# Kernel tuning notes

Measured on AMD Instinct MI355X. Metric: run time of the kernel, lower is better.

The kernel has to match this reference:

```python
import jax, jax.numpy as jnp
import numpy as np

B = 4          # number of point clouds
N = 16384      # points per cloud
RATIO = 0.25
S = int(N * RATIO)   # FPS samples per cloud (fps never duplicates, unique() only sorts)
R = 0.08
K = 32               # max_num_neighbors
BIG = jnp.float32(1e30)


def fps_one(pts):
    """Farthest point sampling on one cloud. pts: [N,3] -> idx [S] (start at 0, random_start=False)."""
    def body(carry, _):
        dists, last = carry
        d = jnp.sum((pts - pts[last]) ** 2, axis=-1)          # [N]
        dists = jnp.minimum(dists, d)
        nxt = jnp.argmax(dists).astype(jnp.int32)
        return (dists, nxt), nxt
    init = (jnp.full((pts.shape[0],), BIG, jnp.float32), jnp.int32(0))
    _, rest = jax.lax.scan(body, init, None, length=S - 1)
    return jnp.concatenate([jnp.zeros((1,), jnp.int32), rest])


def ball_query_one(src, dst):
    """For each dst point pick up to K nearest src points within radius R.
    src: [N,3], dst: [S,3] -> (idx [S,K] int32, valid [S,K] bool)."""
    d2 = jnp.sum((dst[:, None, :] - src[None, :, :]) ** 2, axis=-1)  # [S,N]
    masked = jnp.where(d2 <= R * R, d2, BIG)
    neg_vals, idx = jax.lax.top_k(-masked, K)                        # K smallest distances
    valid = neg_vals > -BIG * 0.5
    return idx.astype(jnp.int32), valid


def setup_inputs() -> dict:
    key = jax.random.key(0)
    k1, _ = jax.random.split(key)
    node_coord_src = jax.random.uniform(k1, (B * N, 3), dtype=jnp.float32)
    batch_src = (jnp.arange(B * N) // N).astype(jnp.int64)
    return {"node_coord_src": node_coord_src, "batch_src": batch_src}


def reference(node_coord_src, batch_src):
    pts = node_coord_src.reshape(B, N, 3)
    # --- FPS + torch.unique (which only sorts, indices are distinct) ---
    fps_idx = jax.vmap(fps_one)(pts)                 # [B,S] local indices
    fps_idx = jnp.sort(fps_idx, axis=-1)
    dst = jnp.take_along_axis(pts, fps_idx[..., None], axis=1)   # [B,S,3]
    # --- radius ball query (padded to K with validity mask) ---
    idx, valid = jax.vmap(ball_query_one)(pts, dst)  # [B,S,K]
    # remove self edges: src local index == fps index of the dst node
    valid = valid & (idx != fps_idx[:, :, None])
    # --- globalize indices and flatten ---
    boff = jnp.arange(B, dtype=jnp.int32)[:, None, None]
    edge_src = (idx + boff * N).reshape(-1)
    edge_dst = jnp.broadcast_to(jnp.arange(S, dtype=jnp.int32)[None, :, None] + boff * S, (B, S, K)).reshape(-1)
    edge_mask = valid.reshape(-1)
    degree = valid.sum(axis=-1).reshape(-1).astype(jnp.int32)    # scatter_add of ones == per-dst count
    node_coord_dst = dst.reshape(-1, 3)
    batch_dst = jnp.repeat(jnp.arange(B, dtype=jnp.int32), S)
    node_dst_idx = (fps_idx + jnp.arange(B, dtype=jnp.int32)[:, None] * N).reshape(-1)
    return (node_coord_dst, edge_src, edge_dst, edge_mask, degree, batch_dst, node_dst_idx)
```

## Files before the change

kernel.cpp:

```cpp
#include <hip/hip_runtime.h>
#include <hip/hip_bf16.h>

constexpr int B = 4;
constexpr int N = 16384;
constexpr int S = 4096;
constexpr int K = 32;
constexpr float BIG = 1e30f;

constexpr size_t OFF_COORD = 0;
constexpr size_t OFF_ESRC  = (size_t)B * S * 3;
constexpr size_t OFF_EDST  = OFF_ESRC + (size_t)B * S * K;
constexpr size_t OFF_MASK  = OFF_EDST + (size_t)B * S * K;
constexpr size_t OFF_DEG   = OFF_MASK + (size_t)B * S * K;
constexpr size_t OFF_BATCH = OFF_DEG + (size_t)B * S;
constexpr size_t OFF_NIDX  = OFF_BATCH + (size_t)B * S;

#define NT_MS 1024
__global__ __launch_bounds__(NT_MS)
void morton_sort_kernel(const float* __restrict__ pts, float4* __restrict__ sbuf) {
    const int b = blockIdx.x, t = threadIdx.x;
    const int lane = t & 63, wave = t >> 6;
    const float* p = pts + (size_t)b * N * 3;
    float4* sb = sbuf + (size_t)b * N;

    __shared__ unsigned int cnt[8192];
    __shared__ int s_wsum[16];

    for (int i = t; i < 8192; i += NT_MS) cnt[i] = 0u;
    __syncthreads();

    float xx[16], yy[16], zz[16];
    int code[16];
#pragma unroll
    for (int j = 0; j < 16; ++j) {
        int i = t + j * NT_MS;
        float x = p[i * 3 + 0], y = p[i * 3 + 1], z = p[i * 3 + 2];
        xx[j] = x; yy[j] = y; zz[j] = z;
        int xi = min(31, (int)(x * 32.0f));
        int yi = min(31, (int)(y * 32.0f));
        int zi = min(15, (int)(z * 16.0f));
        int c = 0;
#pragma unroll
        for (int k = 0; k < 4; ++k) {
            c |= ((zi >> k) & 1) << (3 * k);
            c |= ((yi >> k) & 1) << (3 * k + 1);
            c |= ((xi >> k) & 1) << (3 * k + 2);
        }
        c |= ((xi >> 4) & 1) << 12;
        c |= ((yi >> 4) & 1) << 13;
        code[j] = c;
        atomicAdd(&cnt[c >> 1], (c & 1) ? 0x10000u : 1u);
    }
    __syncthreads();

    unsigned int w[8];
    int tot = 0;
#pragma unroll
    for (int k = 0; k < 8; ++k) {
        w[k] = cnt[t * 8 + k];
        tot += (int)(w[k] & 0xffffu) + (int)(w[k] >> 16);
    }
    int inc = tot;
#pragma unroll
    for (int off = 1; off < 64; off <<= 1) {
        int v = __shfl_up(inc, off);
        if (lane >= off) inc += v;
    }
    if (lane == 63) s_wsum[wave] = inc;
    __syncthreads();
    int wbase = 0;
#pragma unroll
    for (int q = 0; q < 16; ++q) {
        int v = s_wsum[q];
        if (q < wave) wbase += v;
    }
    int excl = wbase + inc - tot;
#pragma unroll
    for (int k = 0; k < 8; ++k) {
        unsigned int c0 = (unsigned int)excl;
        unsigned int c1 = c0 + (w[k] & 0xffffu);
        cnt[t * 8 + k] = c0 | (c1 << 16);
        excl = (int)(c1 + (w[k] >> 16));
    }
    __syncthreads();

#pragma unroll
    for (int j = 0; j < 16; ++j) {
        int i = t + j * NT_MS;
        int c = code[j];
        unsigned int old = atomicAdd(&cnt[c >> 1], (c & 1) ? 0x10000u : 1u);
        int pos = (c & 1) ? (int)(old >> 16) : (int)(old & 0xffffu);
        sb[pos] = make_float4(xx[j], yy[j], zz[j], __int_as_float(i));
    }
}

#define NT_FP 1024
#define CPT 16

__global__ __launch_bounds__(NT_FP, 4)
void fps_pruned_kernel(const float* __restrict__ pts, const float4* __restrict__ sbuf,
                       int* __restrict__ seq) {
    const int b = blockIdx.x, t = threadIdx.x;
    const int lane = t & 63, wave = t >> 6;
    const float* p = pts + (size_t)b * N * 3;
    const float4* sb = sbuf + (size_t)b * N;

    float px[CPT], py[CPT], pz[CPT], dd[CPT];
    unsigned int noi[CPT];
    float blx = BIG, bly = BIG, blz = BIG, bhx = -BIG, bhy = -BIG, bhz = -BIG;
#pragma unroll
    for (int j = 0; j < CPT; ++j) {
        float4 v = sb[t * CPT + j];
        px[j] = v.x; py[j] = v.y; pz[j] = v.z;
        noi[j] = ~(unsigned int)__float_as_int(v.w);
        dd[j] = BIG;
        blx = fminf(blx, v.x); bhx = fmaxf(bhx, v.x);
        bly = fminf(bly, v.y); bhy = fmaxf(bhy, v.y);
        blz = fminf(blz, v.z); bhz = fmaxf(bhz, v.z);
    }
#pragma unroll
    for (int j = 0; j < CPT; ++j)
        asm volatile("" : "+v"(px[j]), "+v"(py[j]), "+v"(pz[j]), "+v"(noi[j]));
    asm volatile("" : "+v"(blx), "+v"(bly), "+v"(blz), "+v"(bhx), "+v"(bhy), "+v"(bhz));

    __shared__ unsigned long long sp[2][NT_FP / 64];

    if (t == 0) seq[b * S + 0] = 0;
    float lx = p[0], ly = p[1], lz = p[2];
    unsigned long long bkey = ((unsigned long long)__float_as_uint(BIG) << 32);

    for (int step = 1; step < S; ++step) {
        float tx = fmaxf(fmaxf(blx - lx, lx - bhx), 0.0f);
        float ty = fmaxf(fmaxf(bly - ly, ly - bhy), 0.0f);
        float tz = fmaxf(fmaxf(blz - lz, lz - bhz), 0.0f);
        float lb = tx * tx + ty * ty + tz * tz;
        float bmax = __uint_as_float((unsigned int)(bkey >> 32));
        if (lb * 0.999998f < bmax) {
            unsigned long long k = 0ull;
#pragma unroll
            for (int j = 0; j < CPT; ++j) {
                float dx = __fsub_rn(px[j], lx);
                float dy = __fsub_rn(py[j], ly);
                float dz = __fsub_rn(pz[j], lz);
                float d  = __fadd_rn(__fadd_rn(__fmul_rn(dx, dx), __fmul_rn(dy, dy)),
                                     __fmul_rn(dz, dz));
                float nd = fminf(dd[j], d);
                dd[j] = nd;
                unsigned long long pk =
                    ((unsigned long long)__float_as_uint(nd) << 32) | noi[j];
                k = (pk > k) ? pk : k;
            }
            bkey = k;
        }
        unsigned long long r = bkey;
#pragma unroll
        for (int off = 32; off >= 1; off >>= 1) {
            unsigned long long o = __shfl_down(r, off);
            r = (o > r) ? o : r;
        }
        if (lane == 0) sp[step & 1][wave] = r;
        __syncthreads();
        unsigned long long g = sp[step & 1][0];
#pragma unroll
        for (int q = 1; q < NT_FP / 64; ++q) {
            unsigned long long o = sp[step & 1][q];
            g = (o > g) ? o : g;
        }
        int wi = (int)(~(unsigned int)g);
        if (t == 0) seq[b * S + step] = wi;
        int wis = __builtin_amdgcn_readfirstlane(wi);
        lx = p[wis * 3 + 0];
        ly = p[wis * 3 + 1];
        lz = p[wis * 3 + 2];
    }
}

#define NT_FPS 512
#define PPT (N / NT_FPS)
#define NWAVE (NT_FPS / 64)
__global__ __launch_bounds__(NT_FPS)
void fps_kernel(const float* __restrict__ pts, int* __restrict__ seq) {
    const int b = blockIdx.x;
    const float* p = pts + (size_t)b * N * 3;
    const int t = threadIdx.x;
    const int lane = t & 63;
    const int wave = t >> 6;
    float px[PPT], py[PPT], pz[PPT], dd[PPT];
    const int base = t * PPT;
#pragma unroll
    for (int j = 0; j < PPT; ++j) {
        px[j] = p[(base + j) * 3 + 0];
        py[j] = p[(base + j) * 3 + 1];
        pz[j] = p[(base + j) * 3 + 2];
        dd[j] = BIG;
    }
#pragma unroll
    for (int j = 0; j < PPT; ++j)
        asm volatile("" : "+v"(px[j]), "+v"(py[j]), "+v"(pz[j]));
    __shared__ unsigned long long s_part[2][NWAVE];
    if (t == 0) seq[b * S + 0] = 0;
    float lx = p[0], ly = p[1], lz = p[2];
    for (int step = 1; step < S; ++step) {
        float bv = -1.0f;
        int bi = 0;
#pragma unroll
        for (int j = 0; j < PPT; ++j) {
            float dx = __fsub_rn(px[j], lx);
            float dy = __fsub_rn(py[j], ly);
            float dz = __fsub_rn(pz[j], lz);
            float d  = __fadd_rn(__fadd_rn(__fmul_rn(dx, dx), __fmul_rn(dy, dy)),
                                 __fmul_rn(dz, dz));
            float nd = fminf(dd[j], d);
            dd[j] = nd;
            if (nd > bv) { bv = nd; bi = base + j; }
        }
        unsigned long long key =
            ((unsigned long long)__float_as_uint(bv) << 32) | (unsigned int)(~bi);
#pragma unroll
        for (int off = 32; off >= 1; off >>= 1) {
            unsigned long long o = __shfl_down(key, off);
            if (o > key) key = o;
        }
        if (lane == 0) s_part[step & 1][wave] = key;
        __syncthreads();
        unsigned long long bk = s_part[step & 1][0];
#pragma unroll
        for (int q = 1; q < NWAVE; ++q) {
            unsigned long long o = s_part[step & 1][q];
            if (o > bk) bk = o;
        }
        int wi = (int)(~(unsigned int)bk);
        if (t == 0) seq[b * S + step] = wi;
        int wis = __builtin_amdgcn_readfirstlane(wi);
        lx = p[wis * 3 + 0];
        ly = p[wis * 3 + 1];
        lz = p[wis * 3 + 2];
    }
}

#define NT_SORT 512
__global__ __launch_bounds__(NT_SORT)
void sort_gather_kernel(const float* __restrict__ pts, const int* __restrict__ seq,
                        int* __restrict__ sorted, float* __restrict__ out) {
    const int b = blockIdx.x;
    const int t = threadIdx.x;
    __shared__ unsigned int bm[N / 32];
    __shared__ int pfx[N / 32];
    __shared__ int s_sorted[S];

    for (int i = t; i < N / 32; i += NT_SORT) bm[i] = 0u;
    __syncthreads();
    for (int i = t; i < S; i += NT_SORT) {
        int v = seq[b * S + i];
        atomicOr(&bm[v >> 5], 1u << (v & 31));
    }
    __syncthreads();

    int myc = __popc(bm[t]);
    pfx[t] = myc;
    __syncthreads();
    for (int off = 1; off < N / 32; off <<= 1) {
        int v = (t >= off) ? pfx[t - off] : 0;
        __syncthreads();
        pfx[t] += v;
        __syncthreads();
    }

    for (int i = t; i < S; i += NT_SORT) {
        int v = seq[b * S + i];
        int w = v >> 5;
        int rank = pfx[w] - __popc(bm[w]) + __popc(bm[w] & ((1u << (v & 31)) - 1u));
        s_sorted[rank] = v;
    }
    __syncthreads();

    for (int r = t; r < S; r += NT_SORT) {
        int v = s_sorted[r];
        int g = b * S + r;
        sorted[g] = v;
        out[OFF_COORD + 3 * (size_t)g + 0] = pts[((size_t)b * N + v) * 3 + 0];
        out[OFF_COORD + 3 * (size_t)g + 1] = pts[((size_t)b * N + v) * 3 + 1];
        out[OFF_COORD + 3 * (size_t)g + 2] = pts[((size_t)b * N + v) * 3 + 2];
        out[OFF_BATCH + g] = (float)b;
        out[OFF_NIDX + g]  = (float)(v + b * N);
    }
}

#define CAP 512
__global__ __launch_bounds__(256)
void ballq_kernel(const float* __restrict__ pts, const int* __restrict__ sorted,
                  float* __restrict__ out) {
    const int w    = threadIdx.x >> 6;
    const int lane = threadIdx.x & 63;
    const int g    = blockIdx.x * 4 + w;
    const int b    = g >> 12;
    const float R2 = (float)(0.08 * 0.08);

    __shared__ float cd2[4][CAP];
    __shared__ int   cidx[4][CAP];
    __shared__ int   coor[4][K];

    const float Dx = out[OFF_COORD + 3 * (size_t)g + 0];
    const float Dy = out[OFF_COORD + 3 * (size_t)g + 1];
    const float Dz = out[OFF_COORD + 3 * (size_t)g + 2];
    const int self = sorted[g];

    const float* p = pts + (size_t)b * N * 3;
    const unsigned long long ltmask = (lane == 63) ? 0x7fffffffffffffffull
                                                   : ((1ull << lane) - 1ull);
    int cnt = 0, oor = 0;
    for (int i0 = 0; i0 < N; i0 += 64) {
        int i = i0 + lane;
        float dx = __fsub_rn(Dx, p[i * 3 + 0]);
        float dy = __fsub_rn(Dy, p[i * 3 + 1]);
        float dz = __fsub_rn(Dz, p[i * 3 + 2]);
        float d2 = __fadd_rn(__fadd_rn(__fmul_rn(dx, dx), __fmul_rn(dy, dy)),
                             __fmul_rn(dz, dz));
        bool in = (d2 <= R2);
        unsigned long long m = __ballot(in);
        if (in) {
            int pos = cnt + __popcll(m & ltmask);
            if (pos < CAP) { cd2[w][pos] = d2; cidx[w][pos] = i; }
        }
        if (oor < K) {
            unsigned long long m2 = ~m;
            if (!in) {
                int p2 = oor + __popcll(m2 & ltmask);
                if (p2 < K) coor[w][p2] = i;
            }
            oor += __popcll(m2);
            if (oor > K) oor = K;
        }
        cnt += __popcll(m);
    }

    const int M  = cnt < CAP ? cnt : CAP;
    const int Mk = M < K ? M : K;
    const size_t eb = (size_t)g * K;
    int deg = 0;
    for (int c = lane; c < M; c += 64) {
        float myd = cd2[w][c];
        int   myi = cidx[w][c];
        int rank = 0;
        for (int j = 0; j < M; ++j) {
            float dj = cd2[w][j];
            int   ij = cidx[w][j];
            rank += (dj < myd || (dj == myd && ij < myi)) ? 1 : 0;
        }
        if (rank < K) {
            bool valid = (myi != self);
            out[OFF_ESRC + eb + rank] = (float)(myi + b * N);
            out[OFF_MASK + eb + rank] = valid ? 1.0f : 0.0f;
            deg += valid ? 1 : 0;
        }
    }
    for (int r = lane; r < K; r += 64) {
        out[OFF_EDST + eb + r] = (float)g;
        if (r >= Mk) {
            out[OFF_ESRC + eb + r] = (float)(coor[w][r - Mk] + b * N);
            out[OFF_MASK + eb + r] = 0.0f;
        }
    }
#pragma unroll
    for (int off = 32; off >= 1; off >>= 1) deg += __shfl_down(deg, off);
    if (lane == 0) out[OFF_DEG + g] = (float)deg;
}

extern "C" void kernel_launch(void* const* d_in, const int* in_sizes, int n_in,
                              void* d_out, int out_size, void* d_ws, size_t ws_size,
                              hipStream_t stream) {
    const float* pts = (const float*)d_in[0];
    float* out = (float*)d_out;

    const size_t sbuf_bytes = (size_t)B * N * sizeof(float4);
    const size_t need = sbuf_bytes + 2 * (size_t)B * S * sizeof(int);

    if (ws_size >= need) {
        float4* sbuf = (float4*)d_ws;
        int* seq    = (int*)((char*)d_ws + sbuf_bytes);
        int* sorted = seq + (size_t)B * S;
        morton_sort_kernel<<<B, NT_MS, 0, stream>>>(pts, sbuf);
        fps_pruned_kernel<<<B, NT_FP, 0, stream>>>(pts, sbuf, seq);
        sort_gather_kernel<<<B, NT_SORT, 0, stream>>>(pts, seq, sorted, out);
        ballq_kernel<<<(B * S) / 4, 256, 0, stream>>>(pts, sorted, out);
    } else {
        int* seq    = (int*)d_ws;
        int* sorted = seq + (size_t)B * S;
        fps_kernel<<<B, NT_FPS, 0, stream>>>(pts, seq);
        sort_gather_kernel<<<B, NT_SORT, 0, stream>>>(pts, seq, sorted, out);
        ballq_kernel<<<(B * S) / 4, 256, 0, stream>>>(pts, sorted, out);
    }
}
```

Before: 5.016 ms.

## Stream FPS point coords from memory instead of registers, skip idle-wave reductions

The pruned FPS kernel no longer keeps each thread's 16 points (x,y,z,index) in registers. It re-reads them as float4 from the sorted buffer whenever the bounding-box test says an update is needed, which cuts register pressure at the cost of repeated global or cache loads per step. Waves where no lane needs an update now skip the shuffle reduction and reuse the cached wave key. The cross-wave final reduction reads the shared partials as 128-bit pairs. The extra memory traffic per step may add latency on the serial critical path.

```diff
diff --git a/kernel.cpp b/kernel.cpp
--- a/kernel.cpp
+++ b/kernel.cpp
@@ -103,31 +103,26 @@
     const int b = blockIdx.x, t = threadIdx.x;
     const int lane = t & 63, wave = t >> 6;
     const float* p = pts + (size_t)b * N * 3;
-    const float4* sb = sbuf + (size_t)b * N;
-
-    float px[CPT], py[CPT], pz[CPT], dd[CPT];
-    unsigned int noi[CPT];
+    const float4* sb = sbuf + (size_t)b * N + (size_t)t * CPT;
+
+    float dd[CPT];
     float blx = BIG, bly = BIG, blz = BIG, bhx = -BIG, bhy = -BIG, bhz = -BIG;
 #pragma unroll
     for (int j = 0; j < CPT; ++j) {
-        float4 v = sb[t * CPT + j];
-        px[j] = v.x; py[j] = v.y; pz[j] = v.z;
-        noi[j] = ~(unsigned int)__float_as_int(v.w);
+        float4 v = sb[j];
         dd[j] = BIG;
         blx = fminf(blx, v.x); bhx = fmaxf(bhx, v.x);
         bly = fminf(bly, v.y); bhy = fmaxf(bhy, v.y);
         blz = fminf(blz, v.z); bhz = fmaxf(bhz, v.z);
     }
-#pragma unroll
-    for (int j = 0; j < CPT; ++j)
-        asm volatile("" : "+v"(px[j]), "+v"(py[j]), "+v"(pz[j]), "+v"(noi[j]));
     asm volatile("" : "+v"(blx), "+v"(bly), "+v"(blz), "+v"(bhx), "+v"(bhy), "+v"(bhz));
 
-    __shared__ unsigned long long sp[2][NT_FP / 64];
+    __shared__ alignas(16) unsigned long long sp[2][NT_FP / 64];
 
     if (t == 0) seq[b * S + 0] = 0;
     float lx = p[0], ly = p[1], lz = p[2];
     unsigned long long bkey = ((unsigned long long)__float_as_uint(BIG) << 32);
+    unsigned long long wkey = bkey;
 
     for (int step = 1; step < S; ++step) {
         float tx = fmaxf(fmaxf(blx - lx, lx - bhx), 0.0f);
@@ -135,36 +130,57 @@
         float tz = fmaxf(fmaxf(blz - lz, lz - bhz), 0.0f);
         float lb = tx * tx + ty * ty + tz * tz;
         float bmax = __uint_as_float((unsigned int)(bkey >> 32));
-        if (lb * 0.999998f < bmax) {
-            unsigned long long k = 0ull;
-#pragma unroll
-            for (int j = 0; j < CPT; ++j) {
-                float dx = __fsub_rn(px[j], lx);
-                float dy = __fsub_rn(py[j], ly);
-                float dz = __fsub_rn(pz[j], lz);
-                float d  = __fadd_rn(__fadd_rn(__fmul_rn(dx, dx), __fmul_rn(dy, dy)),
-                                     __fmul_rn(dz, dz));
-                float nd = fminf(dd[j], d);
-                dd[j] = nd;
-                unsigned long long pk =
-                    ((unsigned long long)__float_as_uint(nd) << 32) | noi[j];
-                k = (pk > k) ? pk : k;
+        bool upd = (lb * 0.999998f < bmax);
+        if (__any(upd)) {
+            if (upd) {
+                unsigned long long k = 0ull;
+#pragma unroll
+                for (int g = 0; g < CPT / 4; ++g) {
+                    float4 v0 = sb[g * 4 + 0];
+                    float4 v1 = sb[g * 4 + 1];
+                    float4 v2 = sb[g * 4 + 2];
+                    float4 v3 = sb[g * 4 + 3];
+#define FPS_PT(V, J)                                                          \
+                    {                                                         \
+                        float dx = __fsub_rn((V).x, lx);                      \
+                        float dy = __fsub_rn((V).y, ly);                      \
+                        float dz = __fsub_rn((V).z, lz);                      \
+                        float d  = __fadd_rn(__fadd_rn(__fmul_rn(dx, dx),     \
+                                   __fmul_rn(dy, dy)), __fmul_rn(dz, dz));    \
+                        float nd = fminf(dd[J], d);                           \
+                        dd[J] = nd;                                           \
+                        unsigned long long pk =                               \
+                            ((unsigned long long)__float_as_uint(nd) << 32) | \
+                            (~(unsigned int)__float_as_int((V).w));           \
+                        k = (pk > k) ? pk : k;                                \
+                    }
+                    FPS_PT(v0, g * 4 + 0)
+                    FPS_PT(v1, g * 4 + 1)
+                    FPS_PT(v2, g * 4 + 2)
+                    FPS_PT(v3, g * 4 + 3)
+#undef FPS_PT
+                    __builtin_amdgcn_sched_barrier(0);
+                }
+                bkey = k;
             }
-            bkey = k;
-        }
-        unsigned long long r = bkey;
-#pragma unroll
-        for (int off = 32; off >= 1; off >>= 1) {
-            unsigned long long o = __shfl_down(r, off);
-            r = (o > r) ? o : r;
-        }
-        if (lane == 0) sp[step & 1][wave] = r;
+            unsigned long long r = bkey;
+#pragma unroll
+            for (int off = 32; off >= 1; off >>= 1) {
+                unsigned long long o = __shfl_down(r, off);
+                r = (o > r) ? o : r;
+            }
+            wkey = r;
+        }
+        if (lane == 0) sp[step & 1][wave] = wkey;
         __syncthreads();
-        unsigned long long g = sp[step & 1][0];
-#pragma unroll
-        for (int q = 1; q < NT_FP / 64; ++q) {
-            unsigned long long o = sp[step & 1][q];
-            g = (o > g) ? o : g;
+
+        const ulonglong2* spp = (const ulonglong2*)(&sp[step & 1][0]);
+        unsigned long long g = 0ull;
+#pragma unroll
+        for (int q = 0; q < NT_FP / 64 / 2; ++q) {
+            ulonglong2 v = spp[q];
+            unsigned long long m = (v.x > v.y) ? v.x : v.y;
+            g = (m > g) ? m : g;
         }
         int wi = (int)(~(unsigned int)g);
         if (t == 0) seq[b * S + step] = wi;
```

Result: slower. 9.521 ms (+89.8%).

## Halve FPS block size, skip wave reductions when all lanes pruned, vectorize LDS reduce

Applied to the files above, without the earlier changes.

The pruned FPS kernel now uses 512 threads with 32 points each instead of 1024 with 16, which halves the number of waves taking part in each step's block-wide max reduction. Each wave skips its distance update and shuffle reduction when no lane's bounding box can beat its current max, reusing the cached wave key. The cross-wave reduction reads the shared-memory keys as 128-bit pairs. A large shared array of 5632 entries per buffer is declared, apparently to limit occupancy and LDS contention. The cost is more registers per thread and more serial work per thread.

```diff
diff --git a/kernel.cpp b/kernel.cpp
--- a/kernel.cpp
+++ b/kernel.cpp
@@ -94,23 +94,26 @@
     }
 }
 
-#define NT_FP 1024
-#define CPT 16
-
-__global__ __launch_bounds__(NT_FP, 4)
+#define NT_FP 512
+#define CPT 32
+#define NW_FP (NT_FP / 64)
+
+__global__ __launch_bounds__(NT_FP, 2)
 void fps_pruned_kernel(const float* __restrict__ pts, const float4* __restrict__ sbuf,
                        int* __restrict__ seq) {
     const int b = blockIdx.x, t = threadIdx.x;
     const int lane = t & 63, wave = t >> 6;
     const float* p = pts + (size_t)b * N * 3;
-    const float4* sb = sbuf + (size_t)b * N;
+    const float4* sb = sbuf + (size_t)b * N + (size_t)t * CPT;
+
+    __shared__ alignas(16) unsigned long long sp[2][5632];
 
     float px[CPT], py[CPT], pz[CPT], dd[CPT];
     unsigned int noi[CPT];
     float blx = BIG, bly = BIG, blz = BIG, bhx = -BIG, bhy = -BIG, bhz = -BIG;
 #pragma unroll
     for (int j = 0; j < CPT; ++j) {
-        float4 v = sb[t * CPT + j];
+        float4 v = sb[j];
         px[j] = v.x; py[j] = v.y; pz[j] = v.z;
         noi[j] = ~(unsigned int)__float_as_int(v.w);
         dd[j] = BIG;
@@ -123,11 +126,10 @@
         asm volatile("" : "+v"(px[j]), "+v"(py[j]), "+v"(pz[j]), "+v"(noi[j]));
     asm volatile("" : "+v"(blx), "+v"(bly), "+v"(blz), "+v"(bhx), "+v"(bhy), "+v"(bhz));
 
-    __shared__ unsigned long long sp[2][NT_FP / 64];
-
     if (t == 0) seq[b * S + 0] = 0;
     float lx = p[0], ly = p[1], lz = p[2];
     unsigned long long bkey = ((unsigned long long)__float_as_uint(BIG) << 32);
+    unsigned long long wkey = bkey;
 
     for (int step = 1; step < S; ++step) {
         float tx = fmaxf(fmaxf(blx - lx, lx - bhx), 0.0f);
@@ -135,36 +137,43 @@
         float tz = fmaxf(fmaxf(blz - lz, lz - bhz), 0.0f);
         float lb = tx * tx + ty * ty + tz * tz;
         float bmax = __uint_as_float((unsigned int)(bkey >> 32));
-        if (lb * 0.999998f < bmax) {
-            unsigned long long k = 0ull;
-#pragma unroll
-            for (int j = 0; j < CPT; ++j) {
-                float dx = __fsub_rn(px[j], lx);
-                float dy = __fsub_rn(py[j], ly);
-                float dz = __fsub_rn(pz[j], lz);
-                float d  = __fadd_rn(__fadd_rn(__fmul_rn(dx, dx), __fmul_rn(dy, dy)),
-                                     __fmul_rn(dz, dz));
-                float nd = fminf(dd[j], d);
-                dd[j] = nd;
-                unsigned long long pk =
-                    ((unsigned long long)__float_as_uint(nd) << 32) | noi[j];
-                k = (pk > k) ? pk : k;
+        bool upd = (lb * 0.999998f < bmax);
+        if (__any(upd)) {
+            if (upd) {
+                unsigned long long k = 0ull;
+#pragma unroll
+                for (int j = 0; j < CPT; ++j) {
+                    float dx = __fsub_rn(px[j], lx);
+                    float dy = __fsub_rn(py[j], ly);
+                    float dz = __fsub_rn(pz[j], lz);
+                    float d  = __fadd_rn(__fadd_rn(__fmul_rn(dx, dx),
+                               __fmul_rn(dy, dy)), __fmul_rn(dz, dz));
+                    float nd = fminf(dd[j], d);
+                    dd[j] = nd;
+                    unsigned long long pk =
+                        ((unsigned long long)__float_as_uint(nd) << 32) | noi[j];
+                    k = (pk > k) ? pk : k;
+                }
+                bkey = k;
             }
-            bkey = k;
-        }
-        unsigned long long r = bkey;
-#pragma unroll
-        for (int off = 32; off >= 1; off >>= 1) {
-            unsigned long long o = __shfl_down(r, off);
-            r = (o > r) ? o : r;
-        }
-        if (lane == 0) sp[step & 1][wave] = r;
+            unsigned long long r = bkey;
+#pragma unroll
+            for (int off = 32; off >= 1; off >>= 1) {
+                unsigned long long o = __shfl_down(r, off);
+                r = (o > r) ? o : r;
+            }
+            wkey = r;
+        }
+        if (lane == 0) sp[step & 1][wave] = wkey;
         __syncthreads();
-        unsigned long long g = sp[step & 1][0];
-#pragma unroll
-        for (int q = 1; q < NT_FP / 64; ++q) {
-            unsigned long long o = sp[step & 1][q];
-            g = (o > g) ? o : g;
+
+        const ulonglong2* spp = (const ulonglong2*)(&sp[step & 1][0]);
+        unsigned long long g = 0ull;
+#pragma unroll
+        for (int q = 0; q < NW_FP / 2; ++q) {
+            ulonglong2 v = spp[q];
+            unsigned long long m = (v.x > v.y) ? v.x : v.y;
+            g = (m > g) ? m : g;
         }
         int wi = (int)(~(unsigned int)g);
         if (t == 0) seq[b * S + step] = wi;
```

Result: slower. 7.559 ms (+50.7%).
